# Kernel tuning notes

Measured on AMD Instinct MI355X. Metric: run time of the kernel, lower is better.

The kernel has to match this reference:

```python
import math
import jax, jax.numpy as jnp
from jax import lax
import numpy as np

E = 16        # num experts
K = 2         # top_k
CF = 1.25     # capacity factor


def setup_inputs() -> dict:
    key = jax.random.key(0)
    k0, k1, k2, k3, k4 = jax.random.split(key, 5)
    B, S, D, H = 2, 2048, 1024, 1024
    scale = 0.02
    return {
        "x": jax.random.normal(k0, (B, S, D), dtype=jnp.float32),
        "router_w": jax.random.normal(k1, (D, E), dtype=jnp.float32) * scale,
        "gate_w": jax.random.normal(k2, (E, D, H), dtype=jnp.float32) * scale,
        "up_w": jax.random.normal(k3, (E, D, H), dtype=jnp.float32) * scale,
        "down_w": jax.random.normal(k4, (E, H, D), dtype=jnp.float32) * scale,
    }


def reference(x, router_w, gate_w, up_w, down_w):
    B, S, D = x.shape
    xf = x.reshape(-1, D)                     # [T, D]
    T = B * S
    capacity = max(1, math.ceil(T * K / E * CF))   # static python int
    Cbuf = K * capacity                       # per-expert buffer (per-column capacity x K)

    # ---- router: softmax over experts, then top-k (weights = top-k probs) ----
    logits = xf @ router_w                    # [T, E]
    probs = jax.nn.softmax(logits, axis=-1)
    w, idx = lax.top_k(probs, K)              # [T, K] each

    # ---- capacity drop: per k-column, per expert, keep first `capacity` tokens ----
    oh = jax.nn.one_hot(idx, E, dtype=w.dtype)            # [T, K, E]
    rank = jnp.cumsum(oh, axis=0) - oh                     # exclusive rank per (k, e)
    myrank = jnp.sum(rank * oh, axis=-1)                   # [T, K]
    keep = myrank < capacity
    w = jnp.where(keep, w, 0.0)

    # ---- dispatch: scatter kept assignments into [E, Cbuf] slots ----
    flat_e = idx.reshape(-1)                               # [A], A = T*K (row-major: token-major)
    flat_w = w.reshape(-1)
    keep_f = keep.reshape(-1)
    tok = jnp.repeat(jnp.arange(T, dtype=jnp.int32), K)    # [A]
    ohk = jax.nn.one_hot(flat_e, E, dtype=jnp.int32) * keep_f[:, None].astype(jnp.int32)
    pos = jnp.cumsum(ohk, axis=0) - ohk                    # exclusive rank among kept per expert
    slot = jnp.sum(pos * ohk, axis=-1)                     # [A], < Cbuf for kept
    e_idx = jnp.where(keep_f, flat_e, E)                   # dropped -> dummy expert row E

    dispatch = jnp.full((E + 1, Cbuf), T, dtype=jnp.int32).at[e_idx, slot].set(tok)
    wbuf = jnp.zeros((E + 1, Cbuf), dtype=w.dtype).at[e_idx, slot].set(flat_w)
    dispatch = dispatch[:E]
    wbuf = wbuf[:E]

    x_pad = jnp.concatenate([xf, jnp.zeros((1, D), xf.dtype)], axis=0)  # sentinel row
    xe = x_pad[dispatch]                                   # [E, Cbuf, D]

    # ---- grouped SwiGLU expert GEMMs ----
    gate = jnp.einsum('ecd,edh->ech', xe, gate_w)
    up = jnp.einsum('ecd,edh->ech', xe, up_w)
    hidden = jax.nn.silu(gate) * up
    out = jnp.einsum('ech,ehd->ecd', hidden, down_w)       # [E, Cbuf, D]
    out = out * wbuf[:, :, None]

    # ---- combine: scatter-add back to tokens ----
    combined = jnp.zeros((T + 1, D), dtype=xf.dtype).at[dispatch.reshape(-1)].add(out.reshape(-1, D))
    return combined[:T].reshape(B, S, D)
```

## Files before the change

kernel.cpp:

```cpp
#include <hip/hip_runtime.h>
#include <math.h>

#define T_TOK 4096
#define DIM   1024
#define HID   1024
#define NE    16
#define CAP   640
#define CBUF  1280
#define BM 128
#define BN 128
#define BK 32
#define MAXTILE 160

typedef __attribute__((ext_vector_type(8))) short short8;
typedef __attribute__((ext_vector_type(4))) float f32x4;

static __device__ __forceinline__ unsigned short f2bf(float f) {
    unsigned int u = __float_as_uint(f);
    u += 0x7fff + ((u >> 16) & 1);
    return (unsigned short)(u >> 16);
}

static __device__ __forceinline__ void async16(const void* g, void* l) {
    __builtin_amdgcn_global_load_lds((const __attribute__((address_space(1))) void*)g,
                                     (__attribute__((address_space(3))) void*)l, 16, 0, 0);
}

__global__ void convert_x_k(const float* __restrict__ x, unsigned short* __restrict__ xb) {
    int i = blockIdx.x * blockDim.x + threadIdx.x;
    int base = i * 4;
    int row = base >> 10;
    ushort4 o;
    if (row < T_TOK) {
        float4 v = *(const float4*)(x + base);
        o.x = f2bf(v.x); o.y = f2bf(v.y); o.z = f2bf(v.z); o.w = f2bf(v.w);
    } else {
        o.x = 0; o.y = 0; o.z = 0; o.w = 0;
    }
    *(ushort4*)(xb + base) = o;
}

#define TSP 68
__global__ void transpose_cvt_k(const float* __restrict__ W0, const float* __restrict__ W1,
                                const float* __restrict__ W2,
                                unsigned short* __restrict__ T0, unsigned short* __restrict__ T1,
                                unsigned short* __restrict__ T2) {
    __shared__ unsigned short s[64 * TSP];
    int zz = blockIdx.z;
    int which = zz >> 4, e = zz & 15;
    const float* W = (which == 0) ? W0 : (which == 1) ? W1 : W2;
    unsigned short* T = (which == 0) ? T0 : (which == 1) ? T1 : T2;
    const float* Wp = W + (size_t)e * DIM * HID;
    unsigned short* Tp = T + (size_t)e * DIM * HID;
    int k0 = blockIdx.y * 64, n0 = blockIdx.x * 64;
    int tid = threadIdx.x;
    int tx = tid & 15, ty = tid >> 4;
    #pragma unroll
    for (int i = 0; i < 4; ++i) {
        int k = ty + i * 16;
        float4 v = *(const float4*)(Wp + (size_t)(k0 + k) * 1024 + n0 + tx * 4);
        int nb = tx * 4;
        s[(nb + 0) * TSP + k] = f2bf(v.x);
        s[(nb + 1) * TSP + k] = f2bf(v.y);
        s[(nb + 2) * TSP + k] = f2bf(v.z);
        s[(nb + 3) * TSP + k] = f2bf(v.w);
    }
    __syncthreads();
    int n = tid >> 2, cseg = (tid & 3) * 16;
    union { ushort4 h[4]; uint4 q[2]; } u;
    #pragma unroll
    for (int j = 0; j < 4; ++j)
        u.h[j] = *(ushort4*)&s[n * TSP + cseg + 4 * j];
    unsigned short* orow = Tp + (size_t)(n0 + n) * 1024 + k0 + cseg;
    *(uint4*)(orow + 0) = u.q[0];
    *(uint4*)(orow + 8) = u.q[1];
}

__global__ void router_k(const float* __restrict__ x, const float* __restrict__ rw,
                         int* __restrict__ route_e, float* __restrict__ route_w) {
    int t = blockIdx.x;
    int lane = threadIdx.x;
    const float* xr = x + (size_t)t * DIM + lane * 16;
    float4 xv0 = *(const float4*)(xr + 0);
    float4 xv1 = *(const float4*)(xr + 4);
    float4 xv2 = *(const float4*)(xr + 8);
    float4 xv3 = *(const float4*)(xr + 12);
    float xl[16] = {xv0.x, xv0.y, xv0.z, xv0.w, xv1.x, xv1.y, xv1.z, xv1.w,
                    xv2.x, xv2.y, xv2.z, xv2.w, xv3.x, xv3.y, xv3.z, xv3.w};
    float p[16];
    #pragma unroll
    for (int e = 0; e < 16; ++e) p[e] = 0.f;
    #pragma unroll
    for (int j = 0; j < 16; ++j) {
        const float4* rp = (const float4*)(rw + (size_t)(lane * 16 + j) * 16);
        float4 r0 = rp[0], r1 = rp[1], r2 = rp[2], r3 = rp[3];
        float xv = xl[j];
        p[0]  += xv * r0.x; p[1]  += xv * r0.y; p[2]  += xv * r0.z; p[3]  += xv * r0.w;
        p[4]  += xv * r1.x; p[5]  += xv * r1.y; p[6]  += xv * r1.z; p[7]  += xv * r1.w;
        p[8]  += xv * r2.x; p[9]  += xv * r2.y; p[10] += xv * r2.z; p[11] += xv * r2.w;
        p[12] += xv * r3.x; p[13] += xv * r3.y; p[14] += xv * r3.z; p[15] += xv * r3.w;
    }
    #pragma unroll
    for (int off = 32; off > 0; off >>= 1) {
        #pragma unroll
        for (int e = 0; e < 16; ++e) p[e] += __shfl_xor(p[e], off);
    }
    if (lane == 0) {
        float m = p[0];
        #pragma unroll
        for (int e = 1; e < 16; ++e) m = fmaxf(m, p[e]);
        float s = 0.f;
        #pragma unroll
        for (int e = 0; e < 16; ++e) s = s + __expf(p[e] - m);
        float v0 = -1e30f, v1 = -1e30f; int i0 = 0, i1 = 0;
        #pragma unroll
        for (int e = 0; e < 16; ++e) {
            float v = p[e];
            if (v > v0)      { v1 = v0; i1 = i0; v0 = v; i0 = e; }
            else if (v > v1) { v1 = v;  i1 = e; }
        }
        route_e[t*2+0] = i0;  route_e[t*2+1] = i1;
        route_w[t*2+0] = __expf(v0 - m) / s;
        route_w[t*2+1] = __expf(v1 - m) / s;
    }
}

__global__ __launch_bounds__(1024)
void build_dispatch_k(const int* __restrict__ route_e, const float* __restrict__ route_w,
                      int* __restrict__ disp, int* __restrict__ smap, int* __restrict__ tmeta) {
    __shared__ unsigned char eidx[2 * T_TOK];
    __shared__ unsigned char keepf[2 * T_TOK];
    __shared__ int totals[NE];
    int tid = threadIdx.x;
    int wv = tid >> 6, lane = tid & 63;

    {
        int4 a = ((const int4*)route_e)[tid * 2];
        int4 b = ((const int4*)route_e)[tid * 2 + 1];
        unsigned int lo = (a.x & 0xff) | ((a.y & 0xff) << 8) | ((a.z & 0xff) << 16) | ((a.w & 0xff) << 24);
        unsigned int hi = (b.x & 0xff) | ((b.y & 0xff) << 8) | ((b.z & 0xff) << 16) | ((b.w & 0xff) << 24);
        uint2 pk; pk.x = lo; pk.y = hi;
        *(uint2*)(eidx + tid * 8) = pk;
    }
    for (int i = tid; i < 2 * T_TOK; i += 1024) smap[i] = -1;
    __syncthreads();

    unsigned long long below = (lane == 0) ? 0ull : ((~0ull) >> (64 - lane));
    #pragma unroll
    for (int s = 0; s < 2; ++s) {
        int st = wv + s * 16;
        int e = st >> 1, k = st & 1;
        int run = 0;
        for (int base = 0; base < T_TOK; base += 64) {
            int t = base + lane;
            int hit = (eidx[t * 2 + k] == e);
            unsigned long long m = __ballot(hit);
            int rank = run + __popcll(m & below);
            if (hit) keepf[t * 2 + k] = (rank < CAP) ? 1 : 0;
            run += __popcll(m);
        }
    }
    __syncthreads();

    {
        int e = wv;
        int run = 0;
        for (int base = 0; base < 2 * T_TOK; base += 64) {
            int f = base + lane;
            int hit = (eidx[f] == e) && keepf[f];
            unsigned long long m = __ballot(hit);
            int slot = run + __popcll(m & below);
            if (hit) {
                disp[e * CBUF + slot] = f >> 1;
                smap[f] = e * CBUF + slot;
            }
            run += __popcll(m);
        }
        if (lane == 0) totals[e] = run;
    }
    __syncthreads();

    for (int i = tid; i < NE * CBUF; i += 1024) {
        int e = i / CBUF, s = i - e * CBUF;
        if (s >= totals[e]) disp[i] = T_TOK;
    }

    if (tid == 0) {
        int n = 0;
        for (int e = 0; e < NE; ++e) {
            int ntl = (totals[e] + BM - 1) / BM;
            for (int m = 0; m < ntl; ++m) { tmeta[4 + n] = (e << 8) | m; ++n; }
        }
        tmeta[0] = n;
    }
}

__global__ __launch_bounds__(256, 2)
void gemm1_k(const unsigned short* __restrict__ xb, const unsigned short* __restrict__ gt,
             const unsigned short* __restrict__ ut, const int* __restrict__ disp,
             const int* __restrict__ tmeta, unsigned short* __restrict__ hidden) {
    int slot = blockIdx.y;
    if (slot >= tmeta[0]) return;
    int pk = tmeta[4 + slot];
    int e = pk >> 8, mt = pk & 255;
    int m0 = mt * BM, n0 = blockIdx.x * BN;

    __shared__ unsigned short As[2 * BM * BK];
    __shared__ unsigned short Bg[2 * BN * BK];
    __shared__ unsigned short Bu[2 * BN * BK];
    __shared__ int tok[BM];
    int tid = threadIdx.x;
    if (tid < BM) tok[tid] = disp[e * CBUF + m0 + tid];
    __syncthreads();

    int lane = tid & 63, w = tid >> 6;
    int cg = (lane & 3) ^ ((lane >> 3) & 3);
    int rl = lane >> 2;
    int rA0 = w * 32 + rl, rA1 = rA0 + 16;
    const unsigned short* srcA0 = xb + (size_t)tok[rA0] * DIM + cg * 8;
    const unsigned short* srcA1 = xb + (size_t)tok[rA1] * DIM + cg * 8;
    const unsigned short* srcG0 = gt + ((size_t)e * HID + n0 + rA0) * DIM + cg * 8;
    const unsigned short* srcG1 = gt + ((size_t)e * HID + n0 + rA1) * DIM + cg * 8;
    const unsigned short* srcU0 = ut + ((size_t)e * HID + n0 + rA0) * DIM + cg * 8;
    const unsigned short* srcU1 = ut + ((size_t)e * HID + n0 + rA1) * DIM + cg * 8;
    unsigned short* dA0 = As + (w * 32) * BK;
    unsigned short* dA1 = As + (w * 32 + 16) * BK;
    unsigned short* dG0 = Bg + (w * 32) * BK;
    unsigned short* dG1 = Bg + (w * 32 + 16) * BK;
    unsigned short* dU0 = Bu + (w * 32) * BK;
    unsigned short* dU1 = Bu + (w * 32 + 16) * BK;

    int wm = w >> 1, wn = w & 1;
    int quad = lane >> 4, ln = lane & 15;
    int swq = quad ^ ((ln >> 1) & 3);

    f32x4 zero4 = {0.f, 0.f, 0.f, 0.f};
    f32x4 accg[4][4], accu[4][4];
    #pragma unroll
    for (int i = 0; i < 4; ++i)
        #pragma unroll
        for (int j = 0; j < 4; ++j) { accg[i][j] = zero4; accu[i][j] = zero4; }

    async16(srcA0, dA0); async16(srcA1, dA1);
    async16(srcG0, dG0); async16(srcG1, dG1);
    async16(srcU0, dU0); async16(srcU1, dU1);

    for (int k0 = 0; k0 < DIM; k0 += BK) {
        int cur = (k0 >> 5) & 1;
        asm volatile("s_waitcnt vmcnt(0)\n\ts_barrier" ::: "memory");
        if (k0 + BK < DIM) {
            int nx = cur ^ 1, nk = k0 + BK;
            async16(srcA0 + nk, dA0 + nx * (BM * BK));
            async16(srcA1 + nk, dA1 + nx * (BM * BK));
            async16(srcG0 + nk, dG0 + nx * (BN * BK));
            async16(srcG1 + nk, dG1 + nx * (BN * BK));
            async16(srcU0 + nk, dU0 + nx * (BN * BK));
            async16(srcU1 + nk, dU1 + nx * (BN * BK));
        }
        const unsigned short* Ab = As + cur * (BM * BK);
        const unsigned short* Gb = Bg + cur * (BN * BK);
        const unsigned short* Ub = Bu + cur * (BN * BK);
        short8 af[4], bgf[4], buf2[4];
        #pragma unroll
        for (int i = 0; i < 4; ++i)
            af[i] = *(const short8*)(Ab + (wm * 64 + i * 16 + ln) * BK + swq * 8);
        #pragma unroll
        for (int j = 0; j < 4; ++j) {
            bgf[j]  = *(const short8*)(Gb + (wn * 64 + j * 16 + ln) * BK + swq * 8);
            buf2[j] = *(const short8*)(Ub + (wn * 64 + j * 16 + ln) * BK + swq * 8);
        }
        #pragma unroll
        for (int i = 0; i < 4; ++i)
            #pragma unroll
            for (int j = 0; j < 4; ++j) {
                accg[i][j] = __builtin_amdgcn_mfma_f32_16x16x32_bf16(af[i], bgf[j],  accg[i][j], 0, 0, 0);
                accu[i][j] = __builtin_amdgcn_mfma_f32_16x16x32_bf16(af[i], buf2[j], accu[i][j], 0, 0, 0);
            }
    }
    #pragma unroll
    for (int i = 0; i < 4; ++i) {
        #pragma unroll
        for (int r = 0; r < 4; ++r) {
            int row = m0 + wm * 64 + i * 16 + quad * 4 + r;
            unsigned short* hrow = hidden + ((size_t)e * CBUF + row) * HID + n0 + wn * 64 + ln;
            #pragma unroll
            for (int j = 0; j < 4; ++j) {
                float g = accg[i][j][r];
                float u = accu[i][j][r];
                float sg = g / (1.f + __expf(-g));
                hrow[j * 16] = f2bf(sg * u);
            }
        }
    }
}

__global__ __launch_bounds__(256, 2)
void gemm2_k(const unsigned short* __restrict__ hidden, const unsigned short* __restrict__ dt,
             const int* __restrict__ tmeta, unsigned short* __restrict__ ebuf) {
    int slot = blockIdx.y;
    if (slot >= tmeta[0]) return;
    int pk = tmeta[4 + slot];
    int e = pk >> 8, mt = pk & 255;
    int m0 = mt * BM, n0 = blockIdx.x * BN;

    __shared__ unsigned short As[2 * BM * BK];
    __shared__ unsigned short Bs[2 * BN * BK];
    int tid = threadIdx.x;

    int lane = tid & 63, w = tid >> 6;
    int cg = (lane & 3) ^ ((lane >> 3) & 3);
    int rl = lane >> 2;
    int rA0 = w * 32 + rl, rA1 = rA0 + 16;
    const unsigned short* srcA0 = hidden + ((size_t)e * CBUF + m0 + rA0) * HID + cg * 8;
    const unsigned short* srcA1 = hidden + ((size_t)e * CBUF + m0 + rA1) * HID + cg * 8;
    const unsigned short* srcB0 = dt + ((size_t)e * DIM + n0 + rA0) * HID + cg * 8;
    const unsigned short* srcB1 = dt + ((size_t)e * DIM + n0 + rA1) * HID + cg * 8;
    unsigned short* dA0 = As + (w * 32) * BK;
    unsigned short* dA1 = As + (w * 32 + 16) * BK;
    unsigned short* dB0 = Bs + (w * 32) * BK;
    unsigned short* dB1 = Bs + (w * 32 + 16) * BK;

    int wm = w >> 1, wn = w & 1;
    int quad = lane >> 4, ln = lane & 15;
    int swq = quad ^ ((ln >> 1) & 3);

    f32x4 zero4 = {0.f, 0.f, 0.f, 0.f};
    f32x4 acc[4][4];
    #pragma unroll
    for (int i = 0; i < 4; ++i)
        #pragma unroll
        for (int j = 0; j < 4; ++j) acc[i][j] = zero4;

    async16(srcA0, dA0); async16(srcA1, dA1);
    async16(srcB0, dB0); async16(srcB1, dB1);

    for (int k0 = 0; k0 < HID; k0 += BK) {
        int cur = (k0 >> 5) & 1;
        asm volatile("s_waitcnt vmcnt(0)\n\ts_barrier" ::: "memory");
        if (k0 + BK < HID) {
            int nx = cur ^ 1, nk = k0 + BK;
            async16(srcA0 + nk, dA0 + nx * (BM * BK));
            async16(srcA1 + nk, dA1 + nx * (BM * BK));
            async16(srcB0 + nk, dB0 + nx * (BN * BK));
            async16(srcB1 + nk, dB1 + nx * (BN * BK));
        }
        const unsigned short* Ab = As + cur * (BM * BK);
        const unsigned short* Bb = Bs + cur * (BN * BK);
        short8 af[4], bf[4];
        #pragma unroll
        for (int i = 0; i < 4; ++i)
            af[i] = *(const short8*)(Ab + (wm * 64 + i * 16 + ln) * BK + swq * 8);
        #pragma unroll
        for (int j = 0; j < 4; ++j)
            bf[j] = *(const short8*)(Bb + (wn * 64 + j * 16 + ln) * BK + swq * 8);
        #pragma unroll
        for (int i = 0; i < 4; ++i)
            #pragma unroll
            for (int j = 0; j < 4; ++j)
                acc[i][j] = __builtin_amdgcn_mfma_f32_16x16x32_bf16(af[i], bf[j], acc[i][j], 0, 0, 0);
    }
    #pragma unroll
    for (int i = 0; i < 4; ++i) {
        #pragma unroll
        for (int r = 0; r < 4; ++r) {
            int row = m0 + wm * 64 + i * 16 + quad * 4 + r;
            unsigned short* erow = ebuf + ((size_t)e * CBUF + row) * DIM + n0 + wn * 64 + ln;
            #pragma unroll
            for (int j = 0; j < 4; ++j)
                erow[j * 16] = f2bf(acc[i][j][r]);
        }
    }
}

__global__ __launch_bounds__(256)
void combine_k(const unsigned short* __restrict__ ebuf, const int* __restrict__ smap,
               const float* __restrict__ rwt, float* __restrict__ out) {
    int t = blockIdx.x * 2 + (threadIdx.x >> 7);
    int c = (threadIdx.x & 127) * 8;
    float acc[8];
    #pragma unroll
    for (int j = 0; j < 8; ++j) acc[j] = 0.f;
    #pragma unroll
    for (int k = 0; k < 2; ++k) {
        int sm = smap[t * 2 + k];
        if (sm >= 0) {
            float wgt = rwt[t * 2 + k];
            uint4 rv = *(const uint4*)(ebuf + (size_t)sm * DIM + c);
            unsigned int d[4] = {rv.x, rv.y, rv.z, rv.w};
            #pragma unroll
            for (int q = 0; q < 4; ++q) {
                acc[q * 2 + 0] += wgt * __uint_as_float(d[q] << 16);
                acc[q * 2 + 1] += wgt * __uint_as_float(d[q] & 0xffff0000u);
            }
        }
    }
    float4 o0 = {acc[0], acc[1], acc[2], acc[3]};
    float4 o1 = {acc[4], acc[5], acc[6], acc[7]};
    float* orow = out + (size_t)t * DIM + c;
    *(float4*)(orow + 0) = o0;
    *(float4*)(orow + 4) = o1;
}

extern "C" void kernel_launch(void* const* d_in, const int* in_sizes, int n_in,
                              void* d_out, int out_size, void* d_ws, size_t ws_size,
                              hipStream_t stream) {
    const float* x  = (const float*)d_in[0];
    const float* rw = (const float*)d_in[1];
    const float* gw = (const float*)d_in[2];
    const float* uw = (const float*)d_in[3];
    const float* dw = (const float*)d_in[4];
    float* out = (float*)d_out;

    char* ws = (char*)d_ws;
    size_t off = 0;
    auto alloc = [&](size_t bytes) { void* p = ws + off; off += (bytes + 255) & ~(size_t)255; return p; };
    unsigned short* xb  = (unsigned short*)alloc((size_t)(T_TOK + 1) * DIM * 2);
    unsigned short* gt  = (unsigned short*)alloc((size_t)NE * DIM * HID * 2);
    unsigned short* ut  = (unsigned short*)alloc((size_t)NE * DIM * HID * 2);
    unsigned short* dtw = (unsigned short*)alloc((size_t)NE * DIM * HID * 2);
    unsigned short* hid = (unsigned short*)alloc((size_t)NE * CBUF * HID * 2);
    int*   disp   = (int*)alloc((size_t)NE * CBUF * 4);
    int*   smap   = (int*)alloc((size_t)T_TOK * 2 * 4);
    int*   tmeta  = (int*)alloc((4 + MAXTILE) * 4);
    int*   re     = (int*)alloc((size_t)T_TOK * 2 * 4);
    float* rwt    = (float*)alloc((size_t)T_TOK * 2 * 4);
    unsigned short* ebuf = gt;
    (void)ws_size; (void)in_sizes; (void)n_in;

    convert_x_k<<<T_TOK + 1, 256, 0, stream>>>(x, xb);
    transpose_cvt_k<<<dim3(16, 16, 48), 256, 0, stream>>>(gw, uw, dw, gt, ut, dtw);
    router_k<<<T_TOK, 64, 0, stream>>>(x, rw, re, rwt);
    build_dispatch_k<<<1, 1024, 0, stream>>>(re, rwt, disp, smap, tmeta);
    gemm1_k<<<dim3(HID / BN, MAXTILE), 256, 0, stream>>>(xb, gt, ut, disp, tmeta, hid);
    gemm2_k<<<dim3(DIM / BN, MAXTILE), 256, 0, stream>>>(hid, dtw, tmeta, ebuf);
    combine_k<<<T_TOK / 2, 256, 0, stream>>>(ebuf, smap, rwt, out);
}
```

Before: 413.1 us.

## Retile expert GEMMs to 128x64x64 single-buffer and widen weight transpose

Both grouped GEMMs move from 128x128 tiles with BK=32 and double-buffered async LDS loads to 128x64 tiles with BK=64, single-buffered, and a new 8-way XOR swizzle. This doubles the grid's N-dimension blocks and halves per-thread accumulators, aiming for higher occupancy and parallelism. The cost is that global loads no longer overlap MFMA work, and there are two barriers per K-step. The weight transpose/convert kernel is also rewritten so each block loops over 256-row K chunks, using fewer, larger blocks with wider stores.

```diff
diff --git a/kernel.cpp b/kernel.cpp
--- a/kernel.cpp
+++ b/kernel.cpp
@@ -8,8 +8,8 @@
 #define CAP   640
 #define CBUF  1280
 #define BM 128
-#define BN 128
-#define BK 32
+#define BN 64
+#define BK 64
 #define MAXTILE 160
 
 typedef __attribute__((ext_vector_type(8))) short short8;
@@ -40,40 +40,54 @@
     *(ushort4*)(xb + base) = o;
 }
 
-#define TSP 68
-__global__ void transpose_cvt_k(const float* __restrict__ W0, const float* __restrict__ W1,
-                                const float* __restrict__ W2,
-                                unsigned short* __restrict__ T0, unsigned short* __restrict__ T1,
-                                unsigned short* __restrict__ T2) {
-    __shared__ unsigned short s[64 * TSP];
+#define TK 256
+#define TST 258
+__global__ __launch_bounds__(256)
+void transpose_cvt_k(const float* __restrict__ W0, const float* __restrict__ W1,
+                     const float* __restrict__ W2,
+                     unsigned short* __restrict__ T0, unsigned short* __restrict__ T1,
+                     unsigned short* __restrict__ T2) {
+    __shared__ unsigned short s[64 * TST];
     int zz = blockIdx.z;
     int which = zz >> 4, e = zz & 15;
     const float* W = (which == 0) ? W0 : (which == 1) ? W1 : W2;
     unsigned short* T = (which == 0) ? T0 : (which == 1) ? T1 : T2;
     const float* Wp = W + (size_t)e * DIM * HID;
     unsigned short* Tp = T + (size_t)e * DIM * HID;
-    int k0 = blockIdx.y * 64, n0 = blockIdx.x * 64;
+    int n0 = blockIdx.x * 64;
     int tid = threadIdx.x;
-    int tx = tid & 15, ty = tid >> 4;
-    #pragma unroll
-    for (int i = 0; i < 4; ++i) {
-        int k = ty + i * 16;
-        float4 v = *(const float4*)(Wp + (size_t)(k0 + k) * 1024 + n0 + tx * 4);
-        int nb = tx * 4;
-        s[(nb + 0) * TSP + k] = f2bf(v.x);
-        s[(nb + 1) * TSP + k] = f2bf(v.y);
-        s[(nb + 2) * TSP + k] = f2bf(v.z);
-        s[(nb + 3) * TSP + k] = f2bf(v.w);
-    }
-    __syncthreads();
-    int n = tid >> 2, cseg = (tid & 3) * 16;
-    union { ushort4 h[4]; uint4 q[2]; } u;
-    #pragma unroll
-    for (int j = 0; j < 4; ++j)
-        u.h[j] = *(ushort4*)&s[n * TSP + cseg + 4 * j];
-    unsigned short* orow = Tp + (size_t)(n0 + n) * 1024 + k0 + cseg;
-    *(uint4*)(orow + 0) = u.q[0];
-    *(uint4*)(orow + 8) = u.q[1];
+    int rsub = tid >> 2;
+    int nofs = (tid & 3) * 16;
+
+    for (int kc = 0; kc < 1024; kc += TK) {
+        #pragma unroll
+        for (int p = 0; p < 4; ++p) {
+            int kl = p * 64 + rsub;
+            const float* rp = Wp + (size_t)(kc + kl) * 1024 + n0 + nofs;
+            float4 v0 = *(const float4*)(rp + 0);
+            float4 v1 = *(const float4*)(rp + 4);
+            float4 v2 = *(const float4*)(rp + 8);
+            float4 v3 = *(const float4*)(rp + 12);
+            float vv[16] = {v0.x, v0.y, v0.z, v0.w, v1.x, v1.y, v1.z, v1.w,
+                            v2.x, v2.y, v2.z, v2.w, v3.x, v3.y, v3.z, v3.w};
+            #pragma unroll
+            for (int v = 0; v < 16; ++v)
+                s[(nofs + v) * TST + kl] = f2bf(vv[v]);
+        }
+        __syncthreads();
+        {
+            int n = tid >> 2;
+            int qo = (tid & 3) * 64;
+            const unsigned short* srow = s + n * TST + qo;
+            unsigned short* orow = Tp + (size_t)(n0 + n) * 1024 + kc + qo;
+            #pragma unroll
+            for (int jj = 0; jj < 8; ++jj) {
+                uint4 o = *(const uint4*)(srow + jj * 8);
+                *(uint4*)(orow + jj * 8) = o;
+            }
+        }
+        __syncthreads();
+    }
 }
 
 __global__ void router_k(const float* __restrict__ x, const float* __restrict__ rw,
@@ -205,86 +219,82 @@
     int e = pk >> 8, mt = pk & 255;
     int m0 = mt * BM, n0 = blockIdx.x * BN;
 
-    __shared__ unsigned short As[2 * BM * BK];
-    __shared__ unsigned short Bg[2 * BN * BK];
-    __shared__ unsigned short Bu[2 * BN * BK];
+    __shared__ unsigned short As[BM * BK];
+    __shared__ unsigned short Bg[BN * BK];
+    __shared__ unsigned short Bu[BN * BK];
     __shared__ int tok[BM];
     int tid = threadIdx.x;
     if (tid < BM) tok[tid] = disp[e * CBUF + m0 + tid];
     __syncthreads();
 
     int lane = tid & 63, w = tid >> 6;
-    int cg = (lane & 3) ^ ((lane >> 3) & 3);
-    int rl = lane >> 2;
-    int rA0 = w * 32 + rl, rA1 = rA0 + 16;
-    const unsigned short* srcA0 = xb + (size_t)tok[rA0] * DIM + cg * 8;
-    const unsigned short* srcA1 = xb + (size_t)tok[rA1] * DIM + cg * 8;
-    const unsigned short* srcG0 = gt + ((size_t)e * HID + n0 + rA0) * DIM + cg * 8;
-    const unsigned short* srcG1 = gt + ((size_t)e * HID + n0 + rA1) * DIM + cg * 8;
-    const unsigned short* srcU0 = ut + ((size_t)e * HID + n0 + rA0) * DIM + cg * 8;
-    const unsigned short* srcU1 = ut + ((size_t)e * HID + n0 + rA1) * DIM + cg * 8;
-    unsigned short* dA0 = As + (w * 32) * BK;
-    unsigned short* dA1 = As + (w * 32 + 16) * BK;
-    unsigned short* dG0 = Bg + (w * 32) * BK;
-    unsigned short* dG1 = Bg + (w * 32 + 16) * BK;
-    unsigned short* dU0 = Bu + (w * 32) * BK;
-    unsigned short* dU1 = Bu + (w * 32 + 16) * BK;
+    int r8 = lane >> 3, c8 = lane & 7;
+    int csw = (c8 ^ r8) * 8;
+
+    const unsigned short* asrc[4];
+    #pragma unroll
+    for (int q = 0; q < 4; ++q)
+        asrc[q] = xb + (size_t)tok[w * 32 + q * 8 + r8] * DIM + csw;
+    const unsigned short* gsrc[2];
+    const unsigned short* usrc[2];
+    #pragma unroll
+    for (int q = 0; q < 2; ++q) {
+        int row = n0 + w * 16 + q * 8 + r8;
+        gsrc[q] = gt + ((size_t)e * HID + row) * DIM + csw;
+        usrc[q] = ut + ((size_t)e * HID + row) * DIM + csw;
+    }
 
     int wm = w >> 1, wn = w & 1;
     int quad = lane >> 4, ln = lane & 15;
-    int swq = quad ^ ((ln >> 1) & 3);
+    int l7 = ln & 7;
 
     f32x4 zero4 = {0.f, 0.f, 0.f, 0.f};
-    f32x4 accg[4][4], accu[4][4];
+    f32x4 accg[4][2], accu[4][2];
     #pragma unroll
     for (int i = 0; i < 4; ++i)
         #pragma unroll
-        for (int j = 0; j < 4; ++j) { accg[i][j] = zero4; accu[i][j] = zero4; }
-
-    async16(srcA0, dA0); async16(srcA1, dA1);
-    async16(srcG0, dG0); async16(srcG1, dG1);
-    async16(srcU0, dU0); async16(srcU1, dU1);
+        for (int j = 0; j < 2; ++j) { accg[i][j] = zero4; accu[i][j] = zero4; }
 
     for (int k0 = 0; k0 < DIM; k0 += BK) {
-        int cur = (k0 >> 5) & 1;
-        asm volatile("s_waitcnt vmcnt(0)\n\ts_barrier" ::: "memory");
-        if (k0 + BK < DIM) {
-            int nx = cur ^ 1, nk = k0 + BK;
-            async16(srcA0 + nk, dA0 + nx * (BM * BK));
-            async16(srcA1 + nk, dA1 + nx * (BM * BK));
-            async16(srcG0 + nk, dG0 + nx * (BN * BK));
-            async16(srcG1 + nk, dG1 + nx * (BN * BK));
-            async16(srcU0 + nk, dU0 + nx * (BN * BK));
-            async16(srcU1 + nk, dU1 + nx * (BN * BK));
-        }
-        const unsigned short* Ab = As + cur * (BM * BK);
-        const unsigned short* Gb = Bg + cur * (BN * BK);
-        const unsigned short* Ub = Bu + cur * (BN * BK);
-        short8 af[4], bgf[4], buf2[4];
-        #pragma unroll
-        for (int i = 0; i < 4; ++i)
-            af[i] = *(const short8*)(Ab + (wm * 64 + i * 16 + ln) * BK + swq * 8);
-        #pragma unroll
-        for (int j = 0; j < 4; ++j) {
-            bgf[j]  = *(const short8*)(Gb + (wn * 64 + j * 16 + ln) * BK + swq * 8);
-            buf2[j] = *(const short8*)(Ub + (wn * 64 + j * 16 + ln) * BK + swq * 8);
-        }
-        #pragma unroll
-        for (int i = 0; i < 4; ++i)
-            #pragma unroll
-            for (int j = 0; j < 4; ++j) {
-                accg[i][j] = __builtin_amdgcn_mfma_f32_16x16x32_bf16(af[i], bgf[j],  accg[i][j], 0, 0, 0);
-                accu[i][j] = __builtin_amdgcn_mfma_f32_16x16x32_bf16(af[i], buf2[j], accu[i][j], 0, 0, 0);
+        #pragma unroll
+        for (int q = 0; q < 4; ++q)
+            async16(asrc[q] + k0, As + (w * 32 + q * 8) * BK);
+        #pragma unroll
+        for (int q = 0; q < 2; ++q) {
+            async16(gsrc[q] + k0, Bg + (w * 16 + q * 8) * BK);
+            async16(usrc[q] + k0, Bu + (w * 16 + q * 8) * BK);
+        }
+        __syncthreads();
+        #pragma unroll
+        for (int kh = 0; kh < 2; ++kh) {
+            int ck = ((quad + 4 * kh) ^ l7) * 8;
+            short8 af[4], bgf[2], buf2[2];
+            #pragma unroll
+            for (int i = 0; i < 4; ++i)
+                af[i] = *(const short8*)(As + (wm * 64 + i * 16 + ln) * BK + ck);
+            #pragma unroll
+            for (int j = 0; j < 2; ++j) {
+                bgf[j]  = *(const short8*)(Bg + (wn * 32 + j * 16 + ln) * BK + ck);
+                buf2[j] = *(const short8*)(Bu + (wn * 32 + j * 16 + ln) * BK + ck);
             }
+            #pragma unroll
+            for (int i = 0; i < 4; ++i)
+                #pragma unroll
+                for (int j = 0; j < 2; ++j) {
+                    accg[i][j] = __builtin_amdgcn_mfma_f32_16x16x32_bf16(af[i], bgf[j],  accg[i][j], 0, 0, 0);
+                    accu[i][j] = __builtin_amdgcn_mfma_f32_16x16x32_bf16(af[i], buf2[j], accu[i][j], 0, 0, 0);
+                }
+        }
+        __syncthreads();
     }
     #pragma unroll
     for (int i = 0; i < 4; ++i) {
         #pragma unroll
         for (int r = 0; r < 4; ++r) {
             int row = m0 + wm * 64 + i * 16 + quad * 4 + r;
-            unsigned short* hrow = hidden + ((size_t)e * CBUF + row) * HID + n0 + wn * 64 + ln;
-            #pragma unroll
-            for (int j = 0; j < 4; ++j) {
+            unsigned short* hrow = hidden + ((size_t)e * CBUF + row) * HID + n0 + wn * 32 + ln;
+            #pragma unroll
+            for (int j = 0; j < 2; ++j) {
                 float g = accg[i][j][r];
                 float u = accu[i][j][r];
                 float sg = g / (1.f + __expf(-g));
@@ -303,70 +313,68 @@
     int e = pk >> 8, mt = pk & 255;
     int m0 = mt * BM, n0 = blockIdx.x * BN;
 
-    __shared__ unsigned short As[2 * BM * BK];
-    __shared__ unsigned short Bs[2 * BN * BK];
+    __shared__ unsigned short As[BM * BK];
+    __shared__ unsigned short Bs[BN * BK];
     int tid = threadIdx.x;
 
     int lane = tid & 63, w = tid >> 6;
-    int cg = (lane & 3) ^ ((lane >> 3) & 3);
-    int rl = lane >> 2;
-    int rA0 = w * 32 + rl, rA1 = rA0 + 16;
-    const unsigned short* srcA0 = hidden + ((size_t)e * CBUF + m0 + rA0) * HID + cg * 8;
-    const unsigned short* srcA1 = hidden + ((size_t)e * CBUF + m0 + rA1) * HID + cg * 8;
-    const unsigned short* srcB0 = dt + ((size_t)e * DIM + n0 + rA0) * HID + cg * 8;
-    const unsigned short* srcB1 = dt + ((size_t)e * DIM + n0 + rA1) * HID + cg * 8;
-    unsigned short* dA0 = As + (w * 32) * BK;
-    unsigned short* dA1 = As + (w * 32 + 16) * BK;
-    unsigned short* dB0 = Bs + (w * 32) * BK;
-    unsigned short* dB1 = Bs + (w * 32 + 16) * BK;
+    int r8 = lane >> 3, c8 = lane & 7;
+    int csw = (c8 ^ r8) * 8;
+
+    const unsigned short* asrc[4];
+    #pragma unroll
+    for (int q = 0; q < 4; ++q)
+        asrc[q] = hidden + ((size_t)e * CBUF + m0 + w * 32 + q * 8 + r8) * HID + csw;
+    const unsigned short* bsrc[2];
+    #pragma unroll
+    for (int q = 0; q < 2; ++q)
+        bsrc[q] = dt + ((size_t)e * DIM + n0 + w * 16 + q * 8 + r8) * HID + csw;
 
     int wm = w >> 1, wn = w & 1;
     int quad = lane >> 4, ln = lane & 15;
-    int swq = quad ^ ((ln >> 1) & 3);
+    int l7 = ln & 7;
 
     f32x4 zero4 = {0.f, 0.f, 0.f, 0.f};
-    f32x4 acc[4][4];
+    f32x4 acc[4][2];
     #pragma unroll
     for (int i = 0; i < 4; ++i)
         #pragma unroll
-        for (int j = 0; j < 4; ++j) acc[i][j] = zero4;
-
-    async16(srcA0, dA0); async16(srcA1, dA1);
-    async16(srcB0, dB0); async16(srcB1, dB1);
+        for (int j = 0; j < 2; ++j) acc[i][j] = zero4;
 
     for (int k0 = 0; k0 < HID; k0 += BK) {
-        int cur = (k0 >> 5) & 1;
-        asm volatile("s_waitcnt vmcnt(0)\n\ts_barrier" ::: "memory");
-        if (k0 + BK < HID) {
-            int nx = cur ^ 1, nk = k0 + BK;
-            async16(srcA0 + nk, dA0 + nx * (BM * BK));
-            async16(srcA1 + nk, dA1 + nx * (BM * BK));
-            async16(srcB0 + nk, dB0 + nx * (BN * BK));
-            async16(srcB1 + nk, dB1 + nx * (BN * BK));
-        }
-        const unsigned short* Ab = As + cur * (BM * BK);
-        const unsigned short* Bb = Bs + cur * (BN * BK);
-        short8 af[4], bf[4];
-        #pragma unroll
-        for (int i = 0; i < 4; ++i)
-            af[i] = *(const short8*)(Ab + (wm * 64 + i * 16 + ln) * BK + swq * 8);
-        #pragma unroll
-        for (int j = 0; j < 4; ++j)
-            bf[j] = *(const short8*)(Bb + (wn * 64 + j * 16 + ln) * BK + swq * 8);
-        #pragma unroll
-        for (int i = 0; i < 4; ++i)
-            #pragma unroll
-            for (int j = 0; j < 4; ++j)
-                acc[i][j] = __builtin_amdgcn_mfma_f32_16x16x32_bf16(af[i], bf[j], acc[i][j], 0, 0, 0);
+        #pragma unroll
+        for (int q = 0; q < 4; ++q)
+            async16(asrc[q] + k0, As + (w * 32 + q * 8) * BK);
+        #pragma unroll
+        for (int q = 0; q < 2; ++q)
+            async16(bsrc[q] + k0, Bs + (w * 16 + q * 8) * BK);
+        __syncthreads();
+        #pragma unroll
+        for (int kh = 0; kh < 2; ++kh) {
+            int ck = ((quad + 4 * kh) ^ l7) * 8;
+            short8 af[4], bf[2];
+            #pragma unroll
+            for (int i = 0; i < 4; ++i)
+                af[i] = *(const short8*)(As + (wm * 64 + i * 16 + ln) * BK + ck);
+            #pragma unroll
+            for (int j = 0; j < 2; ++j)
+                bf[j] = *(const short8*)(Bs + (wn * 32 + j * 16 + ln) * BK + ck);
+            #pragma unroll
+            for (int i = 0; i < 4; ++i)
+                #pragma unroll
+                for (int j = 0; j < 2; ++j)
+                    acc[i][j] = __builtin_amdgcn_mfma_f32_16x16x32_bf16(af[i], bf[j], acc[i][j], 0, 0, 0);
+        }
+        __syncthreads();
     }
     #pragma unroll
     for (int i = 0; i < 4; ++i) {
         #pragma unroll
         for (int r = 0; r < 4; ++r) {
             int row = m0 + wm * 64 + i * 16 + quad * 4 + r;
-            unsigned short* erow = ebuf + ((size_t)e * CBUF + row) * DIM + n0 + wn * 64 + ln;
-            #pragma unroll
-            for (int j = 0; j < 4; ++j)
+            unsigned short* erow = ebuf + ((size_t)e * CBUF + row) * DIM + n0 + wn * 32 + ln;
+            #pragma unroll
+            for (int j = 0; j < 2; ++j)
                 erow[j * 16] = f2bf(acc[i][j][r]);
         }
     }
@@ -428,7 +436,7 @@
     (void)ws_size; (void)in_sizes; (void)n_in;
 
     convert_x_k<<<T_TOK + 1, 256, 0, stream>>>(x, xb);
-    transpose_cvt_k<<<dim3(16, 16, 48), 256, 0, stream>>>(gw, uw, dw, gt, ut, dtw);
+    transpose_cvt_k<<<dim3(16, 1, 48), 256, 0, stream>>>(gw, uw, dw, gt, ut, dtw);
     router_k<<<T_TOK, 64, 0, stream>>>(x, rw, re, rwt);
     build_dispatch_k<<<1, 1024, 0, stream>>>(re, rwt, disp, smap, tmeta);
     gemm1_k<<<dim3(HID / BN, MAXTILE), 256, 0, stream>>>(xb, gt, ut, disp, tmeta, hid);
```

New measurement: 410.9 us. About the same (-0.5%).
